# Optimization experiments

Hardware: AMD Instinct MI355X
Metric: run time of the kernel (lower is better)

Reference implementation:

```python
import jax, jax.numpy as jnp
import numpy as np

B, S, D = 2, 2048, 1024
H = 16
HD = D // H


def setup_inputs() -> dict:
    key = jax.random.key(0)
    k1, k2, k3 = jax.random.split(key, 3)
    x = jax.random.normal(k1, (B, S, D), dtype=jnp.float32)
    # nn.Linear(d, 3d, bias=False): weight [3d, d]; y = x @ W.T
    w_qkv = jax.random.normal(k2, (3 * D, D), dtype=jnp.float32) * (D ** -0.5)
    w_out = jax.random.normal(k3, (D, D), dtype=jnp.float32) * (D ** -0.5)
    return {"x": x, "w_qkv": w_qkv, "w_out": w_out}


def reference(x, w_qkv, w_out):
    batch, seq_len, _ = x.shape
    qkv = jnp.einsum('bsd,ed->bse', x, w_qkv)  # [B,S,3D]
    q, k, v = jnp.split(qkv, 3, axis=-1)
    # [B,S,D] -> [B,H,S,HD]
    def heads(t):
        return t.reshape(batch, seq_len, H, HD).transpose(0, 2, 1, 3)
    q, k, v = heads(q), heads(k), heads(v)
    scale = HD ** -0.5
    attn = jnp.einsum('bhqd,bhkd->bhqk', q, k) * scale  # [B,H,S,S]
    causal = jnp.triu(jnp.ones((seq_len, seq_len), dtype=bool), k=1)
    attn = jnp.where(causal, -jnp.inf, attn)
    attn = jax.nn.softmax(attn, axis=-1)
    out = jnp.einsum('bhqk,bhkd->bhqd', attn, v)  # [B,H,S,HD]
    out = out.transpose(0, 2, 1, 3).reshape(batch, seq_len, D)
    return jnp.einsum('bsd,ed->bse', out, w_out)
```

## Files before the change

kernel.cpp:

```cpp
#include <hip/hip_runtime.h>

#define NUM_B 2
#define SEQ   2048
#define DIM   1024
#define NH    16
#define HD    64

typedef __attribute__((ext_vector_type(8))) short short8;
typedef __attribute__((ext_vector_type(4))) float floatx4;
typedef unsigned short us;

#define SOFTMAX_SHIFT2 17.312340f

__device__ __forceinline__ us f2bf(float f) {
    unsigned u = __float_as_uint(f);
    u += 0x7fffu + ((u >> 16) & 1u);
    return (us)(u >> 16);
}
__device__ __forceinline__ us f2bf_t(float f) {
    return (us)(__float_as_uint(f) >> 16);
}
__device__ __forceinline__ float exp2_raw(float x) {
    float r;
    asm volatile("v_exp_f32 %0, %1" : "=v"(r) : "v"(x));
    return r;
}

#define GLD16(gptr, lptr) __builtin_amdgcn_global_load_lds( \
    (__attribute__((address_space(1))) unsigned int*)(gptr), \
    (__attribute__((address_space(3))) unsigned int*)(lptr), 16, 0, 0)

#define SETP(p) __builtin_amdgcn_s_setprio(p)

__global__ __launch_bounds__(256) void cast_all(
    const float* __restrict__ x, const float* __restrict__ wq,
    const float* __restrict__ wo, us* __restrict__ xb,
    us* __restrict__ wqb, us* __restrict__ wob)
{
    int i = blockIdx.x * 256 + threadIdx.x;
    const float* src; us* dst; int off;
    if (i < 524288)      { src = x;  dst = xb;  off = i; }
    else if (i < 917504) { src = wq; dst = wqb; off = i - 524288; }
    else                 { src = wo; dst = wob; off = i - 917504; }
    const float4* p = (const float4*)src + (size_t)off * 2;
    float4 f0 = p[0];
    float4 f1 = p[1];
    short8 v;
    v[0] = (short)f2bf(f0.x); v[1] = (short)f2bf(f0.y);
    v[2] = (short)f2bf(f0.z); v[3] = (short)f2bf(f0.w);
    v[4] = (short)f2bf(f1.x); v[5] = (short)f2bf(f1.y);
    v[6] = (short)f2bf(f1.z); v[7] = (short)f2bf(f1.w);
    *(short8*)(dst + (size_t)off * 8) = v;
}

__global__ __launch_bounds__(256, 2) void gemm_qkv(
    const us* __restrict__ A, const us* __restrict__ Bw,
    us* __restrict__ qb, us* __restrict__ kb, us* __restrict__ vt)
{
    __shared__ us As[128 * 64];
    __shared__ us Bs[128 * 64];
    const int t = threadIdx.x;
    const int lane = t & 63, w = t >> 6;
    const int l16 = lane & 15, quad = lane >> 4;
    const int wr = (w >> 1) * 64, wc = (w & 1) * 64;
    const int m0 = blockIdx.y * 128, n0 = blockIdx.x * 128;
    const bool isV = (blockIdx.x >= 16);
    const int srow = lane >> 3;
    const int soff = ((lane & 7) ^ srow) << 3;
    const int rsw  = l16 & 7;

    floatx4 acc[4][4];
    #pragma unroll
    for (int i = 0; i < 4; ++i)
        #pragma unroll
        for (int j = 0; j < 4; ++j) acc[i][j] = (floatx4){0.f, 0.f, 0.f, 0.f};

    for (int k0 = 0; k0 < DIM; k0 += 64) {
        #pragma unroll
        for (int c = 0; c < 4; ++c) {
            int chunk = w * 4 + c;
            int row = chunk * 8 + srow;
            GLD16(A  + (size_t)(m0 + row) * DIM + k0 + soff, &As[chunk * 512]);
            GLD16(Bw + (size_t)(n0 + row) * DIM + k0 + soff, &Bs[chunk * 512]);
        }
        __syncthreads();
        #pragma unroll
        for (int s = 0; s < 2; ++s) {
            short8 af[4], bf[4];
            #pragma unroll
            for (int i = 0; i < 4; ++i)
                af[i] = *(const short8*)&As[(wr + i * 16 + l16) * 64 + (((s * 4 + quad) ^ rsw) << 3)];
            #pragma unroll
            for (int j = 0; j < 4; ++j)
                bf[j] = *(const short8*)&Bs[(wc + j * 16 + l16) * 64 + (((s * 4 + quad) ^ rsw) << 3)];
            if (!isV) {
                #pragma unroll
                for (int i = 0; i < 4; ++i)
                    #pragma unroll
                    for (int j = 0; j < 4; ++j)
                        acc[i][j] = __builtin_amdgcn_mfma_f32_16x16x32_bf16(af[i], bf[j], acc[i][j], 0, 0, 0);
            } else {
                #pragma unroll
                for (int i = 0; i < 4; ++i)
                    #pragma unroll
                    for (int j = 0; j < 4; ++j)
                        acc[i][j] = __builtin_amdgcn_mfma_f32_16x16x32_bf16(bf[j], af[i], acc[i][j], 0, 0, 0);
            }
        }
        __syncthreads();
    }

    if (!isV) {
        const int which = n0 >> 10;
        const float sc = (which == 0) ? 0.18033688f : 1.0f;
        us* dst = (which == 0) ? qb : kb;
        #pragma unroll
        for (int i = 0; i < 4; ++i) {
            #pragma unroll
            for (int j = 0; j < 4; ++j) {
                int e = n0 + wc + j * 16 + l16;
                int h  = (e >> 6) & 15;
                int hd = e & 63;
                #pragma unroll
                for (int r = 0; r < 4; ++r) {
                    int m = m0 + wr + i * 16 + quad * 4 + r;
                    int b = m >> 11, s = m & 2047;
                    dst[((size_t)((b * NH + h) * SEQ + s) << 6) + hd] = f2bf(acc[i][j][r] * sc);
                }
            }
        }
    } else {
        #pragma unroll
        for (int i = 0; i < 4; ++i) {
            int m = m0 + wr + i * 16 + l16;
            int b = m >> 11, s = m & 2047;
            #pragma unroll
            for (int j = 0; j < 4; ++j) {
                int e0 = (n0 - 2048) + wc + j * 16 + quad * 4;
                #pragma unroll
                for (int r = 0; r < 4; ++r) {
                    int e = e0 + r;
                    int h = e >> 6, hd = e & 63;
                    vt[((size_t)((b * NH + h) * HD + hd) << 11) + s] = f2bf(acc[i][j][r]);
                }
            }
        }
    }
}

__global__ __launch_bounds__(256, 2) void gemm_out(
    const us* __restrict__ A, const us* __restrict__ Bw, float* __restrict__ outp)
{
    __shared__ us As[64 * 64];
    __shared__ us Bs[128 * 64];
    const int t = threadIdx.x;
    const int lane = t & 63, w = t >> 6;
    const int l16 = lane & 15, quad = lane >> 4;
    const int wr = (w >> 1) * 32, wc = (w & 1) * 64;
    const int m0 = blockIdx.y * 64, n0 = blockIdx.x * 128;
    const int srow = lane >> 3;
    const int soff = ((lane & 7) ^ srow) << 3;
    const int rsw  = l16 & 7;

    floatx4 acc[2][4];
    #pragma unroll
    for (int i = 0; i < 2; ++i)
        #pragma unroll
        for (int j = 0; j < 4; ++j) acc[i][j] = (floatx4){0.f, 0.f, 0.f, 0.f};

    for (int k0 = 0; k0 < DIM; k0 += 64) {
        #pragma unroll
        for (int c = 0; c < 2; ++c) {
            int chunk = w * 2 + c;
            int row = chunk * 8 + srow;
            GLD16(A + (size_t)(m0 + row) * DIM + k0 + soff, &As[chunk * 512]);
        }
        #pragma unroll
        for (int c = 0; c < 4; ++c) {
            int chunk = w * 4 + c;
            int row = chunk * 8 + srow;
            GLD16(Bw + (size_t)(n0 + row) * DIM + k0 + soff, &Bs[chunk * 512]);
        }
        __syncthreads();
        #pragma unroll
        for (int s = 0; s < 2; ++s) {
            short8 af[2], bf[4];
            #pragma unroll
            for (int i = 0; i < 2; ++i)
                af[i] = *(const short8*)&As[(wr + i * 16 + l16) * 64 + (((s * 4 + quad) ^ rsw) << 3)];
            #pragma unroll
            for (int j = 0; j < 4; ++j)
                bf[j] = *(const short8*)&Bs[(wc + j * 16 + l16) * 64 + (((s * 4 + quad) ^ rsw) << 3)];
            #pragma unroll
            for (int i = 0; i < 2; ++i)
                #pragma unroll
                for (int j = 0; j < 4; ++j)
                    acc[i][j] = __builtin_amdgcn_mfma_f32_16x16x32_bf16(af[i], bf[j], acc[i][j], 0, 0, 0);
        }
        __syncthreads();
    }

    #pragma unroll
    for (int i = 0; i < 2; ++i)
        #pragma unroll
        for (int j = 0; j < 4; ++j) {
            int n = n0 + wc + j * 16 + l16;
            #pragma unroll
            for (int r = 0; r < 4; ++r) {
                int m = m0 + wr + i * 16 + quad * 4 + r;
                outp[(size_t)m * DIM + n] = acc[i][j][r];
            }
        }
}

__global__ __launch_bounds__(256, 4) void attn(
    const us* __restrict__ qb, const us* __restrict__ kb,
    const us* __restrict__ vt, us* __restrict__ ob)
{
    __shared__ us Ks[2][64 * 64];
    __shared__ us Vs[2][64 * 64];
    __shared__ us Ps[4 * 16 * 64];
    const int t = threadIdx.x;
    const int lane = t & 63, w = t >> 6;
    const int l16 = lane & 15, quad = lane >> 4;
    const int idx = blockIdx.x;
    const int xcd   = idx & 7;
    const int local = idx >> 3;
    const int bh = (xcd << 2) | (local & 3);
    const int u  = local >> 2;
    int qt;
    if (u < 8)       qt = 31 - u;
    else if (u < 16) qt = u - 8;
    else if (u < 24) qt = 39 - u;
    else             qt = u - 16;
    const int b = bh >> 4, h = bh & 15;
    const int q0 = qt << 6;
    const int r0 = q0 + w * 16;
    const int rowb = r0 + quad * 4;
    const size_t base = (size_t)bh * SEQ * HD;
    const us* qbh = qb + base;
    const us* kbh = kb + base;
    const us* vth = vt + base;
    us* Pp = Ps + w * 16 * 64;
    const int srow = lane >> 3;
    const int soff = ((lane & 7) ^ srow) << 3;
    const int rsw  = l16 & 7;

    short8 qa[2];
    #pragma unroll
    for (int s = 0; s < 2; ++s)
        qa[s] = *(const short8*)(qbh + (size_t)(r0 + l16) * HD + s * 32 + quad * 8);

    floatx4 o[4];
    #pragma unroll
    for (int j = 0; j < 4; ++j) o[j] = (floatx4){0.f, 0.f, 0.f, 0.f};
    float lrow[4] = {0.f, 0.f, 0.f, 0.f};

    #pragma unroll
    for (int c = 0; c < 2; ++c) {
        int chunk = w * 2 + c;
        int row = chunk * 8 + srow;
        GLD16(kbh + (size_t)row * HD + soff, &Ks[0][chunk * 512]);
        GLD16(vth + (size_t)row * SEQ + soff, &Vs[0][chunk * 512]);
    }
    __syncthreads();

    for (int kt = 0; kt <= qt; ++kt) {
        const int cur = kt & 1;
        if (kt < qt) {
            const int j0n = (kt + 1) << 6;
            #pragma unroll
            for (int c = 0; c < 2; ++c) {
                int chunk = w * 2 + c;
                int row = chunk * 8 + srow;
                GLD16(kbh + (size_t)(j0n + row) * HD + soff, &Ks[cur ^ 1][chunk * 512]);
                GLD16(vth + (size_t)row * SEQ + j0n + soff, &Vs[cur ^ 1][chunk * 512]);
            }
        }

        floatx4 sf[4];
        #pragma unroll
        for (int j = 0; j < 4; ++j)
            sf[j] = (floatx4){-SOFTMAX_SHIFT2, -SOFTMAX_SHIFT2, -SOFTMAX_SHIFT2, -SOFTMAX_SHIFT2};
        SETP(1);
        #pragma unroll
        for (int s = 0; s < 2; ++s)
            #pragma unroll
            for (int j = 0; j < 4; ++j) {
                short8 kf = *(const short8*)&Ks[cur][(j * 16 + l16) * 64 + (((s * 4 + quad) ^ rsw) << 3)];
                sf[j] = __builtin_amdgcn_mfma_f32_16x16x32_bf16(qa[s], kf, sf[j], 0, 0, 0);
            }
        SETP(0);

        float p[4][4];
        #pragma unroll
        for (int j = 0; j < 4; ++j)
            #pragma unroll
            for (int r = 0; r < 4; ++r) p[j][r] = sf[j][r];

        if (kt == qt) {
            const int j0 = kt << 6;
            #pragma unroll
            for (int j = 0; j < 4; ++j) {
                int colg = j0 + j * 16 + l16;
                #pragma unroll
                for (int r = 0; r < 4; ++r)
                    if (colg > rowb + r) p[j][r] = -1e30f;
            }
        }

        #pragma unroll
        for (int j = 0; j < 4; ++j) {
            const int gc = j * 2 + (l16 >> 3);
            const int ce = l16 & 7;
            #pragma unroll
            for (int r = 0; r < 4; ++r) {
                p[j][r] = exp2_raw(p[j][r]);
                const int row = quad * 4 + r;
                Pp[row * 64 + ((gc ^ (row & 7)) << 3) + ce] = f2bf_t(p[j][r]);
            }
        }
        #pragma unroll
        for (int r = 0; r < 4; ++r)
            lrow[r] += (p[0][r] + p[1][r]) + (p[2][r] + p[3][r]);

        SETP(1);
        #pragma unroll
        for (int s = 0; s < 2; ++s) {
            short8 pf = *(const short8*)&Pp[l16 * 64 + (((s * 4 + quad) ^ rsw) << 3)];
            #pragma unroll
            for (int j = 0; j < 4; ++j) {
                short8 vf = *(const short8*)&Vs[cur][(j * 16 + l16) * 64 + (((s * 4 + quad) ^ rsw) << 3)];
                o[j] = __builtin_amdgcn_mfma_f32_16x16x32_bf16(pf, vf, o[j], 0, 0, 0);
            }
        }
        SETP(0);
        __syncthreads();
    }

    #pragma unroll
    for (int r = 0; r < 4; ++r) {
        float l = lrow[r];
        l += __shfl_xor(l, 1);
        l += __shfl_xor(l, 2);
        l += __shfl_xor(l, 4);
        l += __shfl_xor(l, 8);
        float inv = 1.0f / l;
        #pragma unroll
        for (int j = 0; j < 4; ++j) {
            float val = o[j][r] * inv;
            ob[(size_t)(b * SEQ + rowb + r) * DIM + h * HD + j * 16 + l16] = f2bf(val);
        }
    }
}

extern "C" void kernel_launch(void* const* d_in, const int* in_sizes, int n_in,
                              void* d_out, int out_size, void* d_ws, size_t ws_size,
                              hipStream_t stream) {
    const float* x     = (const float*)d_in[0];
    const float* w_qkv = (const float*)d_in[1];
    const float* w_out = (const float*)d_in[2];
    float* out = (float*)d_out;
    us* ws = (us*)d_ws;

    const size_t M1 = (size_t)1024 * 1024;
    us* xb  = ws;
    us* wqb = xb  + 4 * M1;
    us* wob = wqb + 3 * M1;
    us* qb  = wob + 1 * M1;
    us* kb  = qb  + 4 * M1;
    us* vt  = kb  + 4 * M1;
    us* obf = vt  + 4 * M1;

    cast_all<<<4096, 256, 0, stream>>>(x, w_qkv, w_out, xb, wqb, wob);
    gemm_qkv<<<dim3(24, 32), 256, 0, stream>>>(xb, wqb, qb, kb, vt);
    attn<<<1024, 256, 0, stream>>>(qb, kb, vt, obf);
    gemm_out<<<dim3(8, 64), 256, 0, stream>>>(obf, wob, out);
}
```

Before: 170.6 us.

## Transpose attention MFMAs and pass P through register shuffles instead of LDS

Swaps the MFMA operand order so S^T and O^T are computed, which puts each query row in a single lane. The softmax probabilities can then be repacked into the PV MFMA operand with cross-lane shuffles, so the per-warp LDS staging buffer for P and its store/load round trip are gone. Row sums become per-lane with a cheaper final reduction, and output stores are vectorized into 4-wide bf16 writes. The cost is extra shuffle and select instructions per tile in exchange for lower LDS traffic and a smaller shared-memory footprint.

After: 175.4 us. +2.8%, slower.

```diff
diff --git a/kernel.cpp b/kernel.cpp
--- a/kernel.cpp
+++ b/kernel.cpp
@@ -8,7 +8,9 @@
 
 typedef __attribute__((ext_vector_type(8))) short short8;
 typedef __attribute__((ext_vector_type(4))) float floatx4;
+typedef __attribute__((ext_vector_type(4))) unsigned short us4;
 typedef unsigned short us;
+typedef unsigned int u32;
 
 #define SOFTMAX_SHIFT2 17.312340f
 
@@ -219,7 +221,6 @@
 {
     __shared__ us Ks[2][64 * 64];
     __shared__ us Vs[2][64 * 64];
-    __shared__ us Ps[4 * 16 * 64];
     const int t = threadIdx.x;
     const int lane = t & 63, w = t >> 6;
     const int l16 = lane & 15, quad = lane >> 4;
@@ -236,15 +237,17 @@
     const int b = bh >> 4, h = bh & 15;
     const int q0 = qt << 6;
     const int r0 = q0 + w * 16;
-    const int rowb = r0 + quad * 4;
+    const int rowq = r0 + l16;
     const size_t base = (size_t)bh * SEQ * HD;
     const us* qbh = qb + base;
     const us* kbh = kb + base;
     const us* vth = vt + base;
-    us* Pp = Ps + w * 16 * 64;
     const int srow = lane >> 3;
     const int soff = ((lane & 7) ^ srow) << 3;
     const int rsw  = l16 & 7;
+    const bool hi = (quad >= 2);
+    const int srcA = l16 + ((quad & 1) << 5);
+    const int srcB = srcA + 16;
 
     short8 qa[2];
     #pragma unroll
@@ -254,7 +257,7 @@
     floatx4 o[4];
     #pragma unroll
     for (int j = 0; j < 4; ++j) o[j] = (floatx4){0.f, 0.f, 0.f, 0.f};
-    float lrow[4] = {0.f, 0.f, 0.f, 0.f};
+    float lsum = 0.f;
 
     #pragma unroll
     for (int c = 0; c < 2; ++c) {
@@ -288,69 +291,63 @@
             #pragma unroll
             for (int j = 0; j < 4; ++j) {
                 short8 kf = *(const short8*)&Ks[cur][(j * 16 + l16) * 64 + (((s * 4 + quad) ^ rsw) << 3)];
-                sf[j] = __builtin_amdgcn_mfma_f32_16x16x32_bf16(qa[s], kf, sf[j], 0, 0, 0);
+                sf[j] = __builtin_amdgcn_mfma_f32_16x16x32_bf16(kf, qa[s], sf[j], 0, 0, 0);
             }
         SETP(0);
 
         float p[4][4];
+        const bool diag = (kt == qt);
+        #pragma unroll
+        for (int j = 0; j < 4; ++j) {
+            const int kg0 = (kt << 6) + j * 16 + quad * 4;
+            #pragma unroll
+            for (int r = 0; r < 4; ++r) {
+                float v = sf[j][r];
+                if (diag && (kg0 + r) > rowq) v = -1e30f;
+                p[j][r] = exp2_raw(v);
+            }
+        }
         #pragma unroll
         for (int j = 0; j < 4; ++j)
-            #pragma unroll
-            for (int r = 0; r < 4; ++r) p[j][r] = sf[j][r];
-
-        if (kt == qt) {
-            const int j0 = kt << 6;
-            #pragma unroll
-            for (int j = 0; j < 4; ++j) {
-                int colg = j0 + j * 16 + l16;
-                #pragma unroll
-                for (int r = 0; r < 4; ++r)
-                    if (colg > rowb + r) p[j][r] = -1e30f;
-            }
-        }
-
-        #pragma unroll
-        for (int j = 0; j < 4; ++j) {
-            const int gc = j * 2 + (l16 >> 3);
-            const int ce = l16 & 7;
-            #pragma unroll
-            for (int r = 0; r < 4; ++r) {
-                p[j][r] = exp2_raw(p[j][r]);
-                const int row = quad * 4 + r;
-                Pp[row * 64 + ((gc ^ (row & 7)) << 3) + ce] = f2bf_t(p[j][r]);
-            }
-        }
-        #pragma unroll
-        for (int r = 0; r < 4; ++r)
-            lrow[r] += (p[0][r] + p[1][r]) + (p[2][r] + p[3][r]);
+            lsum += (p[j][0] + p[j][1]) + (p[j][2] + p[j][3]);
+
+        short8 pf2[2];
+        #pragma unroll
+        for (int el = 0; el < 4; ++el) {
+            u32 w0 = ((u32)f2bf_t(p[1][el]) << 16) | (u32)f2bf_t(p[0][el]);
+            u32 w1 = ((u32)f2bf_t(p[3][el]) << 16) | (u32)f2bf_t(p[2][el]);
+            u32 a0 = (u32)__shfl((int)w0, srcA);
+            u32 b0 = (u32)__shfl((int)w0, srcB);
+            u32 a1 = (u32)__shfl((int)w1, srcA);
+            u32 b1 = (u32)__shfl((int)w1, srcB);
+            pf2[0][el]     = (short)(us)(hi ? (a0 >> 16) : (a0 & 0xffffu));
+            pf2[0][el + 4] = (short)(us)(hi ? (b0 >> 16) : (b0 & 0xffffu));
+            pf2[1][el]     = (short)(us)(hi ? (a1 >> 16) : (a1 & 0xffffu));
+            pf2[1][el + 4] = (short)(us)(hi ? (b1 >> 16) : (b1 & 0xffffu));
+        }
 
         SETP(1);
         #pragma unroll
-        for (int s = 0; s < 2; ++s) {
-            short8 pf = *(const short8*)&Pp[l16 * 64 + (((s * 4 + quad) ^ rsw) << 3)];
+        for (int s = 0; s < 2; ++s)
             #pragma unroll
             for (int j = 0; j < 4; ++j) {
                 short8 vf = *(const short8*)&Vs[cur][(j * 16 + l16) * 64 + (((s * 4 + quad) ^ rsw) << 3)];
-                o[j] = __builtin_amdgcn_mfma_f32_16x16x32_bf16(pf, vf, o[j], 0, 0, 0);
-            }
-        }
+                o[j] = __builtin_amdgcn_mfma_f32_16x16x32_bf16(vf, pf2[s], o[j], 0, 0, 0);
+            }
         SETP(0);
         __syncthreads();
     }
 
-    #pragma unroll
-    for (int r = 0; r < 4; ++r) {
-        float l = lrow[r];
-        l += __shfl_xor(l, 1);
-        l += __shfl_xor(l, 2);
-        l += __shfl_xor(l, 4);
-        l += __shfl_xor(l, 8);
-        float inv = 1.0f / l;
-        #pragma unroll
-        for (int j = 0; j < 4; ++j) {
-            float val = o[j][r] * inv;
-            ob[(size_t)(b * SEQ + rowb + r) * DIM + h * HD + j * 16 + l16] = f2bf(val);
-        }
+    float l = lsum;
+    l += __shfl_xor(l, 16);
+    l += __shfl_xor(l, 32);
+    const float inv = 1.0f / l;
+    #pragma unroll
+    for (int j = 0; j < 4; ++j) {
+        us4 pk;
+        #pragma unroll
+        for (int r = 0; r < 4; ++r) pk[r] = f2bf(o[j][r] * inv);
+        *(us4*)&ob[(size_t)(b * SEQ + rowq) * DIM + h * HD + j * 16 + quad * 4] = pk;
     }
 }
 
```

## Widen attention key tile to 128 columns per iteration

Applied to the files above, without the earlier changes.

The attention kernel now processes 128 keys per loop iteration instead of 64, which halves the number of iterations, barriers and prefetch issues per query tile. K/V/P shared buffers double in size and the V tile gets a new swizzled load layout. Occupancy drops, with launch bounds relaxed to 2 blocks per SM, and register pressure rises from 8 score accumulators. The diagonal tile now wastes compute on fully masked columns when the query tile index is even.

Result: slower. 177.0 us (+3.8%).

```diff
diff --git a/kernel.cpp b/kernel.cpp
--- a/kernel.cpp
+++ b/kernel.cpp
@@ -213,13 +213,13 @@
         }
 }
 
-__global__ __launch_bounds__(256, 4) void attn(
+__global__ __launch_bounds__(256, 2) void attn(
     const us* __restrict__ qb, const us* __restrict__ kb,
     const us* __restrict__ vt, us* __restrict__ ob)
 {
-    __shared__ us Ks[2][64 * 64];
-    __shared__ us Vs[2][64 * 64];
-    __shared__ us Ps[4 * 16 * 64];
+    __shared__ us Ks[2][128 * 64];
+    __shared__ us Vs[2][64 * 128];
+    __shared__ us Ps[4 * 16 * 128];
     const int t = threadIdx.x;
     const int lane = t & 63, w = t >> 6;
     const int l16 = lane & 15, quad = lane >> 4;
@@ -241,9 +241,11 @@
     const us* qbh = qb + base;
     const us* kbh = kb + base;
     const us* vth = vt + base;
-    us* Pp = Ps + w * 16 * 64;
+    us* Pp = Ps + w * 16 * 128;
     const int srow = lane >> 3;
     const int soff = ((lane & 7) ^ srow) << 3;
+    const int vgb  = (l16 ^ quad) << 3;
+    const int vgb2 = (l16 ^ (4 | quad)) << 3;
     const int rsw  = l16 & 7;
 
     short8 qa[2];
@@ -256,81 +258,73 @@
     for (int j = 0; j < 4; ++j) o[j] = (floatx4){0.f, 0.f, 0.f, 0.f};
     float lrow[4] = {0.f, 0.f, 0.f, 0.f};
 
-    #pragma unroll
-    for (int c = 0; c < 2; ++c) {
-        int chunk = w * 2 + c;
-        int row = chunk * 8 + srow;
-        GLD16(kbh + (size_t)row * HD + soff, &Ks[0][chunk * 512]);
-        GLD16(vth + (size_t)row * SEQ + soff, &Vs[0][chunk * 512]);
+    const int T = (qt + 2) >> 1;
+
+    #pragma unroll
+    for (int c = 0; c < 4; ++c) {
+        int chunk = w * 4 + c;
+        GLD16(kbh + (size_t)(chunk * 8 + srow) * HD + soff, &Ks[0][chunk * 512]);
+        GLD16(vth + (size_t)(chunk * 4 + quad) * SEQ + ((chunk & 1) ? vgb2 : vgb),
+              &Vs[0][chunk * 512]);
     }
     __syncthreads();
 
-    for (int kt = 0; kt <= qt; ++kt) {
+    for (int kt = 0; kt < T; ++kt) {
         const int cur = kt & 1;
-        if (kt < qt) {
-            const int j0n = (kt + 1) << 6;
-            #pragma unroll
-            for (int c = 0; c < 2; ++c) {
-                int chunk = w * 2 + c;
-                int row = chunk * 8 + srow;
-                GLD16(kbh + (size_t)(j0n + row) * HD + soff, &Ks[cur ^ 1][chunk * 512]);
-                GLD16(vth + (size_t)row * SEQ + j0n + soff, &Vs[cur ^ 1][chunk * 512]);
-            }
-        }
-
-        floatx4 sf[4];
-        #pragma unroll
-        for (int j = 0; j < 4; ++j)
+        if (kt + 1 < T) {
+            const int j0n = (kt + 1) << 7;
+            #pragma unroll
+            for (int c = 0; c < 4; ++c) {
+                int chunk = w * 4 + c;
+                GLD16(kbh + (size_t)(j0n + chunk * 8 + srow) * HD + soff,
+                      &Ks[cur ^ 1][chunk * 512]);
+                GLD16(vth + (size_t)(chunk * 4 + quad) * SEQ + j0n + ((chunk & 1) ? vgb2 : vgb),
+                      &Vs[cur ^ 1][chunk * 512]);
+            }
+        }
+
+        floatx4 sf[8];
+        #pragma unroll
+        for (int j = 0; j < 8; ++j)
             sf[j] = (floatx4){-SOFTMAX_SHIFT2, -SOFTMAX_SHIFT2, -SOFTMAX_SHIFT2, -SOFTMAX_SHIFT2};
         SETP(1);
         #pragma unroll
         for (int s = 0; s < 2; ++s)
             #pragma unroll
-            for (int j = 0; j < 4; ++j) {
+            for (int j = 0; j < 8; ++j) {
                 short8 kf = *(const short8*)&Ks[cur][(j * 16 + l16) * 64 + (((s * 4 + quad) ^ rsw) << 3)];
                 sf[j] = __builtin_amdgcn_mfma_f32_16x16x32_bf16(qa[s], kf, sf[j], 0, 0, 0);
             }
         SETP(0);
 
-        float p[4][4];
-        #pragma unroll
-        for (int j = 0; j < 4; ++j)
-            #pragma unroll
-            for (int r = 0; r < 4; ++r) p[j][r] = sf[j][r];
-
-        if (kt == qt) {
-            const int j0 = kt << 6;
-            #pragma unroll
-            for (int j = 0; j < 4; ++j) {
-                int colg = j0 + j * 16 + l16;
-                #pragma unroll
-                for (int r = 0; r < 4; ++r)
-                    if (colg > rowb + r) p[j][r] = -1e30f;
-            }
-        }
-
-        #pragma unroll
-        for (int j = 0; j < 4; ++j) {
+        const bool diag = (kt == T - 1);
+        float p[8][4];
+        #pragma unroll
+        for (int j = 0; j < 8; ++j) {
+            const int colg = (kt << 7) + j * 16 + l16;
             const int gc = j * 2 + (l16 >> 3);
             const int ce = l16 & 7;
             #pragma unroll
             for (int r = 0; r < 4; ++r) {
-                p[j][r] = exp2_raw(p[j][r]);
+                float v = sf[j][r];
+                if (diag && colg > rowb + r) v = -1e30f;
+                p[j][r] = exp2_raw(v);
                 const int row = quad * 4 + r;
-                Pp[row * 64 + ((gc ^ (row & 7)) << 3) + ce] = f2bf_t(p[j][r]);
+                Pp[row * 128 + ((gc ^ (row & 7)) << 3) + ce] = f2bf_t(p[j][r]);
             }
         }
         #pragma unroll
         for (int r = 0; r < 4; ++r)
-            lrow[r] += (p[0][r] + p[1][r]) + (p[2][r] + p[3][r]);
+            lrow[r] += ((p[0][r] + p[1][r]) + (p[2][r] + p[3][r]))
+                     + ((p[4][r] + p[5][r]) + (p[6][r] + p[7][r]));
 
         SETP(1);
         #pragma unroll
-        for (int s = 0; s < 2; ++s) {
-            short8 pf = *(const short8*)&Pp[l16 * 64 + (((s * 4 + quad) ^ rsw) << 3)];
+        for (int s = 0; s < 4; ++s) {
+            short8 pf = *(const short8*)&Pp[l16 * 128 + (((s * 4 + quad) ^ rsw) << 3)];
             #pragma unroll
             for (int j = 0; j < 4; ++j) {
-                short8 vf = *(const short8*)&Vs[cur][(j * 16 + l16) * 64 + (((s * 4 + quad) ^ rsw) << 3)];
+                short8 vf = *(const short8*)&Vs[cur][(j * 16 + l16) * 128 + (((s * 4 + quad) ^ rsw) << 3)];
                 o[j] = __builtin_amdgcn_mfma_f32_16x16x32_bf16(pf, vf, o[j], 0, 0, 0);
             }
         }
```
